# Performance work log

Measured on AMD Instinct MI355X. Metric: run time of the kernel, lower is better.

The kernel has to match this reference:

```python
import jax, jax.numpy as jnp
import numpy as np

# Sizes
N, T, P, D = 1000, 4, 10, 13          # nodes, point types, edge types (T*(T+1)/2), basis dim per point
F, H, EA, K, E = 128, 128, 16, 64, 20000  # node feat, edge hidden, edge attr/feat, edge op bottleneck, edges
I_NODE = D * (D + 1) // 2             # 91: symmetric ('ij=ji') self-block irreps dim
I_EDGE = D * D                        # 169: generic ('ij') block irreps dim
AVG_NEIGH = 20.0


def setup_inputs() -> dict:
    ks = jax.random.split(jax.random.key(0), 16)
    Fin = H + 2 * F                   # edge-op input: [edge_msg, node_h_i, node_h_j]
    return {
        'node_feats': jax.random.normal(ks[0], (N, F), jnp.float32),
        'node_attrs': jax.random.uniform(ks[1], (N, T), dtype=jnp.float32),
        'edge_feats': jax.random.normal(ks[2], (E, EA), jnp.float32),
        'edge_attrs': jax.random.normal(ks[3], (E, EA), jnp.float32),
        'edge_index': jax.random.randint(ks[4], (2, E), 0, N),
        'node_types': jax.random.randint(ks[5], (N,), 0, T),
        'edge_types': jax.random.randint(ks[6], (E,), 0, P),
        'W_msg': jax.random.normal(ks[7], (F, F), jnp.float32) / np.float32(np.sqrt(F)),
        'W_attr': jax.random.normal(ks[8], (T, F), jnp.float32) / np.float32(np.sqrt(T)),
        'W_em': jax.random.normal(ks[9], (2 * F + 2 * EA, H), jnp.float32) / np.float32(np.sqrt(2 * F + 2 * EA)),
        'W_proj': jax.random.normal(ks[10], (Fin, K), jnp.float32) / np.float32(np.sqrt(Fin)),
        'W_node': jax.random.normal(ks[11], (T, F, I_NODE), jnp.float32) / np.float32(np.sqrt(F)),
        'W_edge': jax.random.normal(ks[12], (P, K, I_EDGE), jnp.float32) / np.float32(np.sqrt(K)),
        'cob_node': jax.random.normal(ks[13], (T, I_NODE, D, D), jnp.float32) / np.float32(D),
        'cob_edge': jax.random.normal(ks[14], (P, I_EDGE, D, D), jnp.float32) / np.float32(D),
    }


def reference(node_feats, node_attrs, edge_feats, edge_attrs, edge_index, node_types,
              edge_types, W_msg, W_attr, W_em, W_proj, W_node, W_edge, cob_node, cob_edge):
    src, dst = edge_index[0], edge_index[1]
    # --- node message passing (NodeMessageBlock, simplified linear-aggregate form) ---
    m = node_feats @ W_msg                                             # [N, F]
    agg = jax.ops.segment_sum(m[src], dst, num_segments=N) \
        + jax.ops.segment_sum(m[dst], src, num_segments=N)             # symmetric edge list: both dirs
    node_h = node_feats + agg / AVG_NEIGH + node_attrs @ W_attr        # [N, F]
    # --- edge messages (EdgeMessageBlock, simplified) ---
    e_in = jnp.concatenate([node_h[src], node_h[dst], edge_feats, edge_attrs], axis=-1)
    edge_msg = jnp.tanh(e_in @ W_em)                                   # [E, H]
    # --- self-interaction blocks: per-type gather -> op -> einsum('ni,ixy->nxy', ., cob) ---
    node_irred = jnp.einsum('nf,nfi->ni', node_h, W_node[node_types])  # [N, I_NODE]
    node_blocks = jnp.einsum('ni,nixy->nxy', node_irred, cob_node[node_types])  # [N, D, D]
    # --- interaction blocks: per-edge-type op + change of basis, transpose-symmetrized ---
    onehot = jax.nn.one_hot(edge_types, P, dtype=node_feats.dtype)     # [E, P] type selector

    def edge_block(a, b):
        h = jnp.concatenate([edge_msg, a, b], axis=-1) @ W_proj        # [E, K]
        irr = jnp.einsum('epi,ep->ei', jnp.einsum('ek,pki->epi', h, W_edge), onehot)  # [E, I_EDGE]
        return jnp.einsum('epxy,ep->exy', jnp.einsum('ei,pixy->epxy', irr, cob_edge), onehot)  # [E, D, D]

    blk_ij = edge_block(node_h[src], node_h[dst])
    blk_ji = edge_block(node_h[dst], node_h[src])
    edge_blocks = 0.5 * (blk_ij + jnp.swapaxes(blk_ji, -1, -2))        # symm_transpose
    # --- scatter blocks into the dense symmetric block matrix ---
    off = jnp.arange(D)
    nidx = jnp.arange(N)[:, None] * D + off                            # [N, D] diagonal block rows/cols
    rs = src[:, None] * D + off                                        # [E, D]
    cs = dst[:, None] * D + off
    M = jnp.zeros((N * D, N * D), node_feats.dtype)
    M = M.at[nidx[:, :, None], nidx[:, None, :]].add(node_blocks)
    M = M.at[rs[:, :, None], cs[:, None, :]].add(edge_blocks)
    M = M.at[cs[:, :, None], rs[:, None, :]].add(jnp.swapaxes(edge_blocks, -1, -2))
    return M
```

## Files before the change

### kernel.cpp

```cpp
#include <hip/hip_runtime.h>
#include <cmath>

#define NN   1000
#define TT   4
#define PP   10
#define DD   13
#define FF   128
#define HH   128
#define EAA  16
#define KDIM 64
#define EE   20000
#define I_NODE 91
#define I_EDGE 169
#define MROW  13000

__global__ __launch_bounds__(256) void k_zero(float4* __restrict__ p, long n4) {
  long stride = (long)gridDim.x * 256;
  float4 z = make_float4(0.f, 0.f, 0.f, 0.f);
  for (long i = (long)blockIdx.x * 256 + threadIdx.x; i < n4; i += stride)
    p[i] = z;
}

__global__ __launch_bounds__(192) void k_comb(
    const float* __restrict__ We, const float* __restrict__ cobE,
    const float* __restrict__ Wn, const float* __restrict__ cobN,
    float* __restrict__ Wcomb, float* __restrict__ Wnc) {
  int b = blockIdx.x, t = threadIdx.x;
  if (t >= I_EDGE) return;
  if (b < PP * KDIM) {
    int p = b >> 6;
    float acc = 0.f;
    const float* wrow = We + b * I_EDGE;
    const float* crow = cobE + p * I_EDGE * I_EDGE + t;
    for (int i = 0; i < I_EDGE; ++i) acc += wrow[i] * crow[i * I_EDGE];
    Wcomb[b * I_EDGE + t] = acc;
  } else {
    int tf = b - PP * KDIM;
    int ty = tf >> 7;
    float acc = 0.f;
    const float* wrow = Wn + tf * I_NODE;
    const float* crow = cobN + ty * I_NODE * I_EDGE + t;
    for (int i = 0; i < I_NODE; ++i) acc += wrow[i] * crow[i * I_EDGE];
    Wnc[tf * I_EDGE + t] = acc;
  }
}

__global__ __launch_bounds__(128) void k_node_msg(
    const float* __restrict__ nf, const float* __restrict__ Wmsg,
    float* __restrict__ m, float* __restrict__ agg) {
  int n = blockIdx.x, j = threadIdx.x;
  __shared__ float row[FF];
  row[j] = nf[n * FF + j];
  __syncthreads();
  float acc = 0.f;
#pragma unroll 8
  for (int f = 0; f < FF; ++f) acc += row[f] * Wmsg[f * FF + j];
  m[n * FF + j] = acc;
  agg[n * FF + j] = 0.f;
}

__global__ __launch_bounds__(256) void k_scatter(
    const float* __restrict__ m, const int* __restrict__ src,
    const int* __restrict__ dst, float* __restrict__ agg) {
  int idx = blockIdx.x * 256 + threadIdx.x;
  if (idx >= EE * FF) return;
  int e = idx >> 7, j = idx & 127;
  int s = src[e], d = dst[e];
  atomicAdd(&agg[d * FF + j], m[s * FF + j]);
  atomicAdd(&agg[s * FF + j], m[d * FF + j]);
}

__global__ __launch_bounds__(128) void k_node_h(
    const float* __restrict__ nf, const float* __restrict__ agg,
    const float* __restrict__ na, const float* __restrict__ Wattr,
    float* __restrict__ nh) {
  int n = blockIdx.x, j = threadIdx.x;
  float a = 0.f;
#pragma unroll
  for (int t = 0; t < TT; ++t) a += na[n * TT + t] * Wattr[t * FF + j];
  nh[n * FF + j] = nf[n * FF + j] + agg[n * FF + j] * (1.0f / 20.0f) + a;
}

#define EPB 8
__global__ __launch_bounds__(128) void k_edge_msg(
    const float* __restrict__ nh, const float* __restrict__ ef,
    const float* __restrict__ ea, const int* __restrict__ src,
    const int* __restrict__ dst, const float* __restrict__ Wem,
    float* __restrict__ emsg) {
  int e0 = blockIdx.x * EPB;
  int j = threadIdx.x;
  __shared__ float xin[EPB][2 * FF + 2 * EAA];
  for (int e = 0; e < EPB; ++e) {
    int ee = e0 + e;
    int s = src[ee], d = dst[ee];
    for (int i = j; i < 288; i += 128) {
      float v;
      if (i < 128)      v = nh[s * FF + i];
      else if (i < 256) v = nh[d * FF + (i - 128)];
      else if (i < 272) v = ef[ee * EAA + (i - 256)];
      else              v = ea[ee * EAA + (i - 272)];
      xin[e][i] = v;
    }
  }
  __syncthreads();
  float acc[EPB];
#pragma unroll
  for (int e = 0; e < EPB; ++e) acc[e] = 0.f;
  for (int c = 0; c < 288; c += 4) {
    float4 xv[EPB];
#pragma unroll
    for (int e = 0; e < EPB; ++e) xv[e] = *(const float4*)&xin[e][c];
#pragma unroll
    for (int sub = 0; sub < 4; ++sub) {
      float w = Wem[(c + sub) * HH + j];
#pragma unroll
      for (int e = 0; e < EPB; ++e) {
        float x = (sub == 0) ? xv[e].x : (sub == 1) ? xv[e].y : (sub == 2) ? xv[e].z : xv[e].w;
        acc[e] += x * w;
      }
    }
  }
#pragma unroll
  for (int e = 0; e < EPB; ++e) emsg[(e0 + e) * HH + j] = tanhf(acc[e]);
}

__global__ __launch_bounds__(192) void k_node_block(
    const float* __restrict__ nh, const int* __restrict__ ntype,
    const float* __restrict__ Wnc, float* __restrict__ M) {
  int n = blockIdx.x, t = threadIdx.x;
  int ty = ntype[n];
  __shared__ float row[FF];
  if (t < FF) row[t] = nh[n * FF + t];
  __syncthreads();
  if (t < I_EDGE) {
    float acc = 0.f;
    const float* W = Wnc + ty * FF * I_EDGE + t;
#pragma unroll 4
    for (int f = 0; f < FF; ++f) acc += row[f] * W[f * I_EDGE];
    int x = t / DD, y = t % DD;
    M[(size_t)(n * DD + x) * MROW + (n * DD + y)] = acc;
  }
}

#define E2 2
__global__ __launch_bounds__(256) void k_edge_blk(
    const float* __restrict__ nh, const float* __restrict__ emsg,
    const int* __restrict__ src, const int* __restrict__ dst,
    const int* __restrict__ etype, const float* __restrict__ Wproj,
    const float* __restrict__ Wcomb, float* __restrict__ M) {
  int e0 = blockIdx.x * E2;
  int t = threadIdx.x;
  __shared__ float xin[E2][384];
  __shared__ float hp[4][256];
  __shared__ float hv[4][KDIM];
  __shared__ float tji[E2][I_EDGE];
  __shared__ int se[E2], de[E2], pe[E2];

  if (t < E2) {
    int e = e0 + t;
    se[t] = src[e]; de[t] = dst[e]; pe[t] = etype[e];
  }
  __syncthreads();
  for (int e = 0; e < E2; ++e) {
    int ee = e0 + e, s = se[e], d = de[e];
    if (t < 128) {
      xin[e][t] = emsg[ee * HH + t];
      xin[e][256 + t] = nh[d * FF + t];
    } else {
      xin[e][t] = nh[s * FF + (t - 128)];
    }
  }
  __syncthreads();

  {
    int k = t & 63, seg = t >> 6;
    float a0 = 0.f, a1 = 0.f, a2 = 0.f, a3 = 0.f;
    const float* Wp = Wproj + k;
    int i0 = seg * 96;
    for (int c = i0; c < i0 + 96; c += 4) {
      int cs = (c < 128) ? c : (c < 256 ? c + 128 : c - 128);
      float4 x0 = *(const float4*)&xin[0][c];
      float4 x0s = *(const float4*)&xin[0][cs];
      float4 x1 = *(const float4*)&xin[1][c];
      float4 x1s = *(const float4*)&xin[1][cs];
      float w0 = Wp[(c + 0) * KDIM], w1 = Wp[(c + 1) * KDIM];
      float w2 = Wp[(c + 2) * KDIM], w3 = Wp[(c + 3) * KDIM];
      a0 += x0.x * w0 + x0.y * w1 + x0.z * w2 + x0.w * w3;
      a1 += x0s.x * w0 + x0s.y * w1 + x0s.z * w2 + x0s.w * w3;
      a2 += x1.x * w0 + x1.y * w1 + x1.z * w2 + x1.w * w3;
      a3 += x1s.x * w0 + x1s.y * w1 + x1s.z * w2 + x1s.w * w3;
    }
    hp[0][t] = a0; hp[1][t] = a1; hp[2][t] = a2; hp[3][t] = a3;
  }
  __syncthreads();
  if (t < KDIM) {
#pragma unroll
    for (int q = 0; q < 4; ++q)
      hv[q][t] = hp[q][t] + hp[q][t + 64] + hp[q][t + 128] + hp[q][t + 192];
  }
  __syncthreads();

  float b0 = 0.f, b1 = 0.f, b2 = 0.f, b3 = 0.f;
  if (t < I_EDGE) {
    const float* W0 = Wcomb + pe[0] * KDIM * I_EDGE + t;
    const float* W1 = Wcomb + pe[1] * KDIM * I_EDGE + t;
    for (int k = 0; k < KDIM; k += 4) {
      float4 h0 = *(const float4*)&hv[0][k];
      float4 h1 = *(const float4*)&hv[1][k];
      float4 h2 = *(const float4*)&hv[2][k];
      float4 h3 = *(const float4*)&hv[3][k];
      float u0 = W0[(k + 0) * I_EDGE], u1 = W0[(k + 1) * I_EDGE];
      float u2 = W0[(k + 2) * I_EDGE], u3 = W0[(k + 3) * I_EDGE];
      float v0 = W1[(k + 0) * I_EDGE], v1 = W1[(k + 1) * I_EDGE];
      float v2 = W1[(k + 2) * I_EDGE], v3 = W1[(k + 3) * I_EDGE];
      b0 += h0.x * u0 + h0.y * u1 + h0.z * u2 + h0.w * u3;
      b1 += h1.x * u0 + h1.y * u1 + h1.z * u2 + h1.w * u3;
      b2 += h2.x * v0 + h2.y * v1 + h2.z * v2 + h2.w * v3;
      b3 += h3.x * v0 + h3.y * v1 + h3.z * v2 + h3.w * v3;
    }
    tji[0][t] = b1; tji[1][t] = b3;
  }
  __syncthreads();

  if (t < I_EDGE) {
    int x = t / DD, y = t % DD;
    int tr = y * DD + x;
    {
      int s = se[0], d = de[0];
      float eb = 0.5f * (b0 + tji[0][tr]);
      atomicAdd(&M[(size_t)(s * DD + x) * MROW + (d * DD + y)], eb);
      atomicAdd(&M[(size_t)(d * DD + y) * MROW + (s * DD + x)], eb);
    }
    {
      int s = se[1], d = de[1];
      float eb = 0.5f * (b2 + tji[1][tr]);
      atomicAdd(&M[(size_t)(s * DD + x) * MROW + (d * DD + y)], eb);
      atomicAdd(&M[(size_t)(d * DD + y) * MROW + (s * DD + x)], eb);
    }
  }
}

extern "C" void kernel_launch(void* const* d_in, const int* in_sizes, int n_in,
                              void* d_out, int out_size, void* d_ws, size_t ws_size,
                              hipStream_t stream) {
  const float* node_feats = (const float*)d_in[0];
  const float* node_attrs = (const float*)d_in[1];
  const float* edge_feats = (const float*)d_in[2];
  const float* edge_attrs = (const float*)d_in[3];
  const int*   edge_index = (const int*)d_in[4];
  const int*   node_types = (const int*)d_in[5];
  const int*   edge_types = (const int*)d_in[6];
  const float* W_msg  = (const float*)d_in[7];
  const float* W_attr = (const float*)d_in[8];
  const float* W_em   = (const float*)d_in[9];
  const float* W_proj = (const float*)d_in[10];
  const float* W_node = (const float*)d_in[11];
  const float* W_edge = (const float*)d_in[12];
  const float* cob_node = (const float*)d_in[13];
  const float* cob_edge = (const float*)d_in[14];

  float* M  = (float*)d_out;
  float* ws = (float*)d_ws;
  float* m_buf = ws;
  float* agg   = ws + 128000;
  float* nh    = ws + 256000;
  float* emsg  = ws + 384000;
  float* Wcomb = ws + 2944000;
  float* Wnc   = ws + 3052160;

  const int* src = edge_index;
  const int* dst = edge_index + EE;

  long n4 = (long)out_size / 4;
  k_zero      <<<4096, 256, 0, stream>>>((float4*)M, n4);
  k_comb      <<<PP * KDIM + TT * FF, 192, 0, stream>>>(W_edge, cob_edge, W_node, cob_node, Wcomb, Wnc);
  k_node_msg  <<<NN, 128, 0, stream>>>(node_feats, W_msg, m_buf, agg);
  k_scatter   <<<(EE * FF) / 256, 256, 0, stream>>>(m_buf, src, dst, agg);
  k_node_h    <<<NN, 128, 0, stream>>>(node_feats, agg, node_attrs, W_attr, nh);
  k_edge_msg  <<<EE / EPB, 128, 0, stream>>>(nh, edge_feats, edge_attrs, src, dst, W_em, emsg);
  k_node_block<<<NN, 192, 0, stream>>>(nh, node_types, Wnc, M);
  k_edge_blk  <<<EE / E2, 256, 0, stream>>>(nh, emsg, src, dst, edge_types,
                                            W_proj, Wcomb, M);
}
```

Baseline: 962.3 us.

## Fuse output zeroing into early compute kernels and skip duplicate shared loads

Drops the standalone zero-fill kernel and splits zeroing of the large output matrix into slices written by the node-message, scatter, node-h and edge-message kernels. The aim is to overlap the bandwidth-bound memset with the latency- and atomic-bound small kernels and remove one launch. The edge-block projection also reuses the same float4 when the swapped operand is identical, cutting shared-memory reads. The risk is that the slice sizes are hard-coded and must sum exactly to the output size, and that heavier fills may slow kernels that had little work of their own.

```diff
diff --git a/kernel.cpp b/kernel.cpp
--- a/kernel.cpp
+++ b/kernel.cpp
@@ -14,11 +14,13 @@
 #define I_EDGE 169
 #define MROW  13000
 
-__global__ __launch_bounds__(256) void k_zero(float4* __restrict__ p, long n4) {
-  long stride = (long)gridDim.x * 256;
+__device__ __forceinline__ void fill_slice(float4* __restrict__ Mz, long zbase,
+                                           long zn, int nthr) {
+  long stride = (long)gridDim.x * nthr;
   float4 z = make_float4(0.f, 0.f, 0.f, 0.f);
-  for (long i = (long)blockIdx.x * 256 + threadIdx.x; i < n4; i += stride)
-    p[i] = z;
+  for (long i = zbase + (long)blockIdx.x * nthr + threadIdx.x; i < zbase + zn;
+       i += stride)
+    Mz[i] = z;
 }
 
 __global__ __launch_bounds__(192) void k_comb(
@@ -47,7 +49,9 @@
 
 __global__ __launch_bounds__(128) void k_node_msg(
     const float* __restrict__ nf, const float* __restrict__ Wmsg,
-    float* __restrict__ m, float* __restrict__ agg) {
+    float* __restrict__ m, float* __restrict__ agg,
+    float4* __restrict__ Mz, long zbase, long zn) {
+  fill_slice(Mz, zbase, zn, 128);
   int n = blockIdx.x, j = threadIdx.x;
   __shared__ float row[FF];
   row[j] = nf[n * FF + j];
@@ -61,7 +65,9 @@
 
 __global__ __launch_bounds__(256) void k_scatter(
     const float* __restrict__ m, const int* __restrict__ src,
-    const int* __restrict__ dst, float* __restrict__ agg) {
+    const int* __restrict__ dst, float* __restrict__ agg,
+    float4* __restrict__ Mz, long zbase, long zn) {
+  fill_slice(Mz, zbase, zn, 256);
   int idx = blockIdx.x * 256 + threadIdx.x;
   if (idx >= EE * FF) return;
   int e = idx >> 7, j = idx & 127;
@@ -73,7 +79,8 @@
 __global__ __launch_bounds__(128) void k_node_h(
     const float* __restrict__ nf, const float* __restrict__ agg,
     const float* __restrict__ na, const float* __restrict__ Wattr,
-    float* __restrict__ nh) {
+    float* __restrict__ nh, float4* __restrict__ Mz, long zbase, long zn) {
+  fill_slice(Mz, zbase, zn, 128);
   int n = blockIdx.x, j = threadIdx.x;
   float a = 0.f;
 #pragma unroll
@@ -86,7 +93,8 @@
     const float* __restrict__ nh, const float* __restrict__ ef,
     const float* __restrict__ ea, const int* __restrict__ src,
     const int* __restrict__ dst, const float* __restrict__ Wem,
-    float* __restrict__ emsg) {
+    float* __restrict__ emsg, float4* __restrict__ Mz, long zbase, long zn) {
+  fill_slice(Mz, zbase, zn, 128);
   int e0 = blockIdx.x * EPB;
   int j = threadIdx.x;
   __shared__ float xin[EPB][2 * FF + 2 * EAA];
@@ -178,11 +186,15 @@
     const float* Wp = Wproj + k;
     int i0 = seg * 96;
     for (int c = i0; c < i0 + 96; c += 4) {
-      int cs = (c < 128) ? c : (c < 256 ? c + 128 : c - 128);
       float4 x0 = *(const float4*)&xin[0][c];
-      float4 x0s = *(const float4*)&xin[0][cs];
       float4 x1 = *(const float4*)&xin[1][c];
-      float4 x1s = *(const float4*)&xin[1][cs];
+      float4 x0s, x1s;
+      if (c < 128) { x0s = x0; x1s = x1; }
+      else {
+        int cs = (c < 256) ? c + 128 : c - 128;
+        x0s = *(const float4*)&xin[0][cs];
+        x1s = *(const float4*)&xin[1][cs];
+      }
       float w0 = Wp[(c + 0) * KDIM], w1 = Wp[(c + 1) * KDIM];
       float w2 = Wp[(c + 2) * KDIM], w3 = Wp[(c + 3) * KDIM];
       a0 += x0.x * w0 + x0.y * w1 + x0.z * w2 + x0.w * w3;
@@ -260,6 +272,7 @@
   const float* cob_edge = (const float*)d_in[14];
 
   float* M  = (float*)d_out;
+  float4* M4 = (float4*)d_out;
   float* ws = (float*)d_ws;
   float* m_buf = ws;
   float* agg   = ws + 128000;
@@ -272,12 +285,16 @@
   const int* dst = edge_index + EE;
 
   long n4 = (long)out_size / 4;
-  k_zero      <<<4096, 256, 0, stream>>>((float4*)M, n4);
+  long z1 = 3000000;
+  long z2 = 18000000;
+  long z3 = 3000000;
+  long z4 = n4 - z1 - z2 - z3;
+
   k_comb      <<<PP * KDIM + TT * FF, 192, 0, stream>>>(W_edge, cob_edge, W_node, cob_node, Wcomb, Wnc);
-  k_node_msg  <<<NN, 128, 0, stream>>>(node_feats, W_msg, m_buf, agg);
-  k_scatter   <<<(EE * FF) / 256, 256, 0, stream>>>(m_buf, src, dst, agg);
-  k_node_h    <<<NN, 128, 0, stream>>>(node_feats, agg, node_attrs, W_attr, nh);
-  k_edge_msg  <<<EE / EPB, 128, 0, stream>>>(nh, edge_feats, edge_attrs, src, dst, W_em, emsg);
+  k_node_msg  <<<NN, 128, 0, stream>>>(node_feats, W_msg, m_buf, agg, M4, 0, z1);
+  k_scatter   <<<(EE * FF) / 256, 256, 0, stream>>>(m_buf, src, dst, agg, M4, z1, z2);
+  k_node_h    <<<NN, 128, 0, stream>>>(node_feats, agg, node_attrs, W_attr, nh, M4, z1 + z2, z3);
+  k_edge_msg  <<<EE / EPB, 128, 0, stream>>>(nh, edge_feats, edge_attrs, src, dst, W_em, emsg, M4, z1 + z2 + z3, z4);
   k_node_block<<<NN, 192, 0, stream>>>(nh, node_types, Wnc, M);
   k_edge_blk  <<<EE / E2, 256, 0, stream>>>(nh, emsg, src, dst, edge_types,
                                             W_proj, Wcomb, M);
```

Result: slower. 1.255 ms (+30.4%).

## Factor W_proj per node, bucket edges by type, fold transpose into weights

Applied to the files above, without the earlier changes.

Splits the edge projection into per-node precomputed terms (B1/B2 from node_h) plus a per-edge term from edge_msg, so the node-feature part of the 384-wide projection is done once per node instead of twice per edge. The symmetric transpose averaging is folded into a concatenated weight matrix Wcat that holds both the direct and transposed combined weights, scaled by 0.5. Edges are bucketed by type with atomic counters so each output block handles 8 edges sharing one weight slice and reuses weights across them. The zero kernel is changed to one element per thread. This adds several kernels and an Hcat round trip through global memory. Bucket capacity is fixed at 2560 edges per type, so overflow edges would be dropped.

```diff
diff --git a/kernel.cpp b/kernel.cpp
--- a/kernel.cpp
+++ b/kernel.cpp
@@ -13,27 +13,39 @@
 #define I_NODE 91
 #define I_EDGE 169
 #define MROW  13000
+#define BCAP 2560
+#define EOB  8
+#define CHUNK (BCAP / EOB)
 
 __global__ __launch_bounds__(256) void k_zero(float4* __restrict__ p, long n4) {
-  long stride = (long)gridDim.x * 256;
-  float4 z = make_float4(0.f, 0.f, 0.f, 0.f);
-  for (long i = (long)blockIdx.x * 256 + threadIdx.x; i < n4; i += stride)
-    p[i] = z;
+  long i = (long)blockIdx.x * 256 + threadIdx.x;
+  if (i < n4) p[i] = make_float4(0.f, 0.f, 0.f, 0.f);
+}
+
+__global__ void k_setup(int* __restrict__ cnt) {
+  if (threadIdx.x < PP) cnt[threadIdx.x] = 0;
 }
 
 __global__ __launch_bounds__(192) void k_comb(
     const float* __restrict__ We, const float* __restrict__ cobE,
     const float* __restrict__ Wn, const float* __restrict__ cobN,
-    float* __restrict__ Wcomb, float* __restrict__ Wnc) {
+    float* __restrict__ Wcat, float* __restrict__ Wnc) {
   int b = blockIdx.x, t = threadIdx.x;
   if (t >= I_EDGE) return;
+  int x = t / DD, y = t % DD;
+  int tr = y * DD + x;
   if (b < PP * KDIM) {
-    int p = b >> 6;
-    float acc = 0.f;
+    int p = b >> 6, k = b & 63;
+    float a = 0.f, c = 0.f;
     const float* wrow = We + b * I_EDGE;
-    const float* crow = cobE + p * I_EDGE * I_EDGE + t;
-    for (int i = 0; i < I_EDGE; ++i) acc += wrow[i] * crow[i * I_EDGE];
-    Wcomb[b * I_EDGE + t] = acc;
+    const float* cbase = cobE + p * I_EDGE * I_EDGE;
+    for (int i = 0; i < I_EDGE; ++i) {
+      float w = wrow[i];
+      a += w * cbase[i * I_EDGE + t];
+      c += w * cbase[i * I_EDGE + tr];
+    }
+    Wcat[(size_t)(p * 128 + k) * I_EDGE + t] = 0.5f * a;
+    Wcat[(size_t)(p * 128 + 64 + k) * I_EDGE + t] = 0.5f * c;
   } else {
     int tf = b - PP * KDIM;
     int ty = tf >> 7;
@@ -68,6 +80,15 @@
   int s = src[e], d = dst[e];
   atomicAdd(&agg[d * FF + j], m[s * FF + j]);
   atomicAdd(&agg[s * FF + j], m[d * FF + j]);
+}
+
+__global__ __launch_bounds__(256) void k_bucket(
+    const int* __restrict__ etype, int* __restrict__ cnt, int* __restrict__ list) {
+  int e = blockIdx.x * 256 + threadIdx.x;
+  if (e >= EE) return;
+  int p = etype[e];
+  int r = atomicAdd(&cnt[p], 1);
+  if (r < BCAP) list[p * BCAP + r] = e;
 }
 
 __global__ __launch_bounds__(128) void k_node_h(
@@ -124,6 +145,49 @@
   for (int e = 0; e < EPB; ++e) emsg[(e0 + e) * HH + j] = tanhf(acc[e]);
 }
 
+__global__ __launch_bounds__(128) void k_nodeproj(
+    const float* __restrict__ nh, const float* __restrict__ Wproj,
+    float* __restrict__ B1, float* __restrict__ B2) {
+  int n = blockIdx.x, t = threadIdx.x;
+  __shared__ float row[FF];
+  row[t] = nh[n * FF + t];
+  __syncthreads();
+  int half = t >> 6, k = t & 63;
+  const float* W = Wproj + (FF + half * FF) * KDIM + k;
+  float acc = 0.f;
+#pragma unroll 4
+  for (int i = 0; i < FF; ++i) acc += row[i] * W[i * KDIM];
+  (half ? B2 : B1)[n * KDIM + k] = acc;
+}
+
+__global__ __launch_bounds__(256) void k_hmsg(
+    const float* __restrict__ emsg, const int* __restrict__ src,
+    const int* __restrict__ dst, const float* __restrict__ Wproj,
+    const float* __restrict__ B1, const float* __restrict__ B2,
+    float* __restrict__ Hcat) {
+  int blk = blockIdx.x, t = threadIdx.x;
+  int e_loc = t >> 6, k = t & 63;
+  __shared__ float xm[4][HH];
+  __shared__ int sL[4], dL[4];
+  if (t < 4) {
+    int e = blk * 4 + t;
+    sL[t] = src[e]; dL[t] = dst[e];
+  }
+  for (int i = t; i < 4 * HH; i += 256)
+    xm[i >> 7][i & 127] = emsg[(blk * 4 + (i >> 7)) * HH + (i & 127)];
+  __syncthreads();
+  float acc = 0.f;
+  const float* Wp = Wproj + k;
+  for (int c = 0; c < HH; c += 4) {
+    float4 xv = *(const float4*)&xm[e_loc][c];
+    acc += xv.x * Wp[(c + 0) * KDIM] + xv.y * Wp[(c + 1) * KDIM]
+         + xv.z * Wp[(c + 2) * KDIM] + xv.w * Wp[(c + 3) * KDIM];
+  }
+  int e = blk * 4 + e_loc, s = sL[e_loc], d = dL[e_loc];
+  Hcat[(size_t)e * 128 + k]      = acc + B1[s * KDIM + k] + B2[d * KDIM + k];
+  Hcat[(size_t)e * 128 + 64 + k] = acc + B1[d * KDIM + k] + B2[s * KDIM + k];
+}
+
 __global__ __launch_bounds__(192) void k_node_block(
     const float* __restrict__ nh, const int* __restrict__ ntype,
     const float* __restrict__ Wnc, float* __restrict__ M) {
@@ -142,101 +206,53 @@
   }
 }
 
-#define E2 2
-__global__ __launch_bounds__(256) void k_edge_blk(
-    const float* __restrict__ nh, const float* __restrict__ emsg,
-    const int* __restrict__ src, const int* __restrict__ dst,
-    const int* __restrict__ etype, const float* __restrict__ Wproj,
-    const float* __restrict__ Wcomb, float* __restrict__ M) {
-  int e0 = blockIdx.x * E2;
+__global__ __launch_bounds__(256) void k_edge_out(
+    const float* __restrict__ Hcat, const int* __restrict__ src,
+    const int* __restrict__ dst, const int* __restrict__ cnt,
+    const int* __restrict__ list, const float* __restrict__ Wcat,
+    float* __restrict__ M) {
+  int p = blockIdx.x / CHUNK;
+  int base = (blockIdx.x % CHUNK) * EOB;
+  int ecnt = cnt[p]; if (ecnt > BCAP) ecnt = BCAP;
+  if (base >= ecnt) return;
+  int nval = ecnt - base; if (nval > EOB) nval = EOB;
   int t = threadIdx.x;
-  __shared__ float xin[E2][384];
-  __shared__ float hp[4][256];
-  __shared__ float hv[4][KDIM];
-  __shared__ float tji[E2][I_EDGE];
-  __shared__ int se[E2], de[E2], pe[E2];
-
-  if (t < E2) {
-    int e = e0 + t;
-    se[t] = src[e]; de[t] = dst[e]; pe[t] = etype[e];
-  }
-  __syncthreads();
-  for (int e = 0; e < E2; ++e) {
-    int ee = e0 + e, s = se[e], d = de[e];
-    if (t < 128) {
-      xin[e][t] = emsg[ee * HH + t];
-      xin[e][256 + t] = nh[d * FF + t];
-    } else {
-      xin[e][t] = nh[s * FF + (t - 128)];
+
+  __shared__ float4 hv4[EOB][32];
+  __shared__ int eL[EOB], sL[EOB], dL[EOB];
+  if (t < EOB) {
+    int slot = (t < nval) ? t : 0;
+    int e = list[p * BCAP + base + slot];
+    eL[t] = e; sL[t] = src[e]; dL[t] = dst[e];
+  }
+  __syncthreads();
+  {
+    int e_loc = t >> 5, q = t & 31;
+    hv4[e_loc][q] = ((const float4*)(Hcat + (size_t)eL[e_loc] * 128))[q];
+  }
+  __syncthreads();
+
+  if (t >= I_EDGE) return;
+  float acc[EOB];
+#pragma unroll
+  for (int e = 0; e < EOB; ++e) acc[e] = 0.f;
+  const float* W = Wcat + (size_t)p * 128 * I_EDGE + t;
+  for (int k4 = 0; k4 < 32; ++k4) {
+    float w0 = W[(k4 * 4 + 0) * I_EDGE];
+    float w1 = W[(k4 * 4 + 1) * I_EDGE];
+    float w2 = W[(k4 * 4 + 2) * I_EDGE];
+    float w3 = W[(k4 * 4 + 3) * I_EDGE];
+#pragma unroll
+    for (int e = 0; e < EOB; ++e) {
+      float4 h = hv4[e][k4];
+      acc[e] += h.x * w0 + h.y * w1 + h.z * w2 + h.w * w3;
     }
   }
-  __syncthreads();
-
-  {
-    int k = t & 63, seg = t >> 6;
-    float a0 = 0.f, a1 = 0.f, a2 = 0.f, a3 = 0.f;
-    const float* Wp = Wproj + k;
-    int i0 = seg * 96;
-    for (int c = i0; c < i0 + 96; c += 4) {
-      int cs = (c < 128) ? c : (c < 256 ? c + 128 : c - 128);
-      float4 x0 = *(const float4*)&xin[0][c];
-      float4 x0s = *(const float4*)&xin[0][cs];
-      float4 x1 = *(const float4*)&xin[1][c];
-      float4 x1s = *(const float4*)&xin[1][cs];
-      float w0 = Wp[(c + 0) * KDIM], w1 = Wp[(c + 1) * KDIM];
-      float w2 = Wp[(c + 2) * KDIM], w3 = Wp[(c + 3) * KDIM];
-      a0 += x0.x * w0 + x0.y * w1 + x0.z * w2 + x0.w * w3;
-      a1 += x0s.x * w0 + x0s.y * w1 + x0s.z * w2 + x0s.w * w3;
-      a2 += x1.x * w0 + x1.y * w1 + x1.z * w2 + x1.w * w3;
-      a3 += x1s.x * w0 + x1s.y * w1 + x1s.z * w2 + x1s.w * w3;
-    }
-    hp[0][t] = a0; hp[1][t] = a1; hp[2][t] = a2; hp[3][t] = a3;
-  }
-  __syncthreads();
-  if (t < KDIM) {
-#pragma unroll
-    for (int q = 0; q < 4; ++q)
-      hv[q][t] = hp[q][t] + hp[q][t + 64] + hp[q][t + 128] + hp[q][t + 192];
-  }
-  __syncthreads();
-
-  float b0 = 0.f, b1 = 0.f, b2 = 0.f, b3 = 0.f;
-  if (t < I_EDGE) {
-    const float* W0 = Wcomb + pe[0] * KDIM * I_EDGE + t;
-    const float* W1 = Wcomb + pe[1] * KDIM * I_EDGE + t;
-    for (int k = 0; k < KDIM; k += 4) {
-      float4 h0 = *(const float4*)&hv[0][k];
-      float4 h1 = *(const float4*)&hv[1][k];
-      float4 h2 = *(const float4*)&hv[2][k];
-      float4 h3 = *(const float4*)&hv[3][k];
-      float u0 = W0[(k + 0) * I_EDGE], u1 = W0[(k + 1) * I_EDGE];
-      float u2 = W0[(k + 2) * I_EDGE], u3 = W0[(k + 3) * I_EDGE];
-      float v0 = W1[(k + 0) * I_EDGE], v1 = W1[(k + 1) * I_EDGE];
-      float v2 = W1[(k + 2) * I_EDGE], v3 = W1[(k + 3) * I_EDGE];
-      b0 += h0.x * u0 + h0.y * u1 + h0.z * u2 + h0.w * u3;
-      b1 += h1.x * u0 + h1.y * u1 + h1.z * u2 + h1.w * u3;
-      b2 += h2.x * v0 + h2.y * v1 + h2.z * v2 + h2.w * v3;
-      b3 += h3.x * v0 + h3.y * v1 + h3.z * v2 + h3.w * v3;
-    }
-    tji[0][t] = b1; tji[1][t] = b3;
-  }
-  __syncthreads();
-
-  if (t < I_EDGE) {
-    int x = t / DD, y = t % DD;
-    int tr = y * DD + x;
-    {
-      int s = se[0], d = de[0];
-      float eb = 0.5f * (b0 + tji[0][tr]);
-      atomicAdd(&M[(size_t)(s * DD + x) * MROW + (d * DD + y)], eb);
-      atomicAdd(&M[(size_t)(d * DD + y) * MROW + (s * DD + x)], eb);
-    }
-    {
-      int s = se[1], d = de[1];
-      float eb = 0.5f * (b2 + tji[1][tr]);
-      atomicAdd(&M[(size_t)(s * DD + x) * MROW + (d * DD + y)], eb);
-      atomicAdd(&M[(size_t)(d * DD + y) * MROW + (s * DD + x)], eb);
-    }
+  int x = t / DD, y = t % DD;
+  for (int i = 0; i < nval; ++i) {
+    int s = sL[i], d = dL[i];
+    atomicAdd(&M[(size_t)(s * DD + x) * MROW + (d * DD + y)], acc[i]);
+    atomicAdd(&M[(size_t)(d * DD + y) * MROW + (s * DD + x)], acc[i]);
   }
 }
 
@@ -265,20 +281,28 @@
   float* agg   = ws + 128000;
   float* nh    = ws + 256000;
   float* emsg  = ws + 384000;
-  float* Wcomb = ws + 2944000;
-  float* Wnc   = ws + 3052160;
+  float* Hcat  = ws + 2944000;
+  float* B1    = ws + 5504000;
+  float* B2    = ws + 5568000;
+  float* Wcat  = ws + 5632000;
+  float* Wnc   = ws + 5848320;
+  int*   cnt   = (int*)(ws + 5934848);
+  int*   list  = cnt + 16;
 
   const int* src = edge_index;
   const int* dst = edge_index + EE;
 
   long n4 = (long)out_size / 4;
-  k_zero      <<<4096, 256, 0, stream>>>((float4*)M, n4);
-  k_comb      <<<PP * KDIM + TT * FF, 192, 0, stream>>>(W_edge, cob_edge, W_node, cob_node, Wcomb, Wnc);
+  k_zero      <<<(int)((n4 + 255) / 256), 256, 0, stream>>>((float4*)M, n4);
+  k_setup     <<<1, 64, 0, stream>>>(cnt);
+  k_comb      <<<PP * KDIM + TT * FF, 192, 0, stream>>>(W_edge, cob_edge, W_node, cob_node, Wcat, Wnc);
+  k_bucket    <<<(EE + 255) / 256, 256, 0, stream>>>(edge_types, cnt, list);
   k_node_msg  <<<NN, 128, 0, stream>>>(node_feats, W_msg, m_buf, agg);
   k_scatter   <<<(EE * FF) / 256, 256, 0, stream>>>(m_buf, src, dst, agg);
   k_node_h    <<<NN, 128, 0, stream>>>(node_feats, agg, node_attrs, W_attr, nh);
   k_edge_msg  <<<EE / EPB, 128, 0, stream>>>(nh, edge_feats, edge_attrs, src, dst, W_em, emsg);
+  k_nodeproj  <<<NN, 128, 0, stream>>>(nh, W_proj, B1, B2);
+  k_hmsg      <<<EE / 4, 256, 0, stream>>>(emsg, src, dst, W_proj, B1, B2, Hcat);
   k_node_block<<<NN, 192, 0, stream>>>(nh, node_types, Wnc, M);
-  k_edge_blk  <<<EE / E2, 256, 0, stream>>>(nh, emsg, src, dst, edge_types,
-                                            W_proj, Wcomb, M);
-}
+  k_edge_out  <<<PP * CHUNK, 256, 0, stream>>>(Hcat, src, dst, cnt, list, Wcat, M);
+}
```

After: 1.012 ms. +5.1%, slower.
